# Optimization experiments

Hardware: AMD Instinct MI355X
Metric: run time of the kernel (lower is better)

The kernel has to match this reference:

```python
import jax, jax.numpy as jnp
import numpy as np

DIM = 1024
HEADS = 16
HEAD_DIM = DIM // HEADS
SCALE = 1.0 / np.sqrt(HEAD_DIM).astype(np.float32)


def setup_inputs() -> dict:
    key = jax.random.key(0)
    ks = jax.random.split(key, 5)
    B, N, C = 2, 2048, DIM
    x = jax.random.normal(ks[0], (B, N, C), dtype=jnp.float32)
    w_qkv = jax.random.normal(ks[1], (C, 3 * C), dtype=jnp.float32) * (1.0 / np.sqrt(C))
    b_qkv = jax.random.normal(ks[2], (3 * C,), dtype=jnp.float32) * 0.02
    w_proj = jax.random.normal(ks[3], (C, C), dtype=jnp.float32) * (1.0 / np.sqrt(C))
    b_proj = jax.random.normal(ks[4], (C,), dtype=jnp.float32) * 0.02
    return {"x": x, "w_qkv": w_qkv, "b_qkv": b_qkv, "w_proj": w_proj, "b_proj": b_proj}


def reference(x, w_qkv, b_qkv, w_proj, b_proj):
    B, N, C = x.shape
    H, D = HEADS, C // HEADS
    # fused QKV projection: [B,N,3C] -> [3,B,H,N,D]
    qkv = (x @ w_qkv + b_qkv).reshape(B, N, 3, H, D).transpose(2, 0, 3, 1, 4)
    q, k, v = qkv[0], qkv[1], qkv[2]
    # scores [B,H,N,N]
    scores = jnp.einsum("bhnd,bhmd->bhnm", q, k) * SCALE
    attn = jax.nn.softmax(scores, axis=-1)
    # attention output -> [B,N,C]
    y = jnp.einsum("bhnm,bhmd->bhnd", attn, v).transpose(0, 2, 1, 3).reshape(B, N, C)
    return y @ w_proj + b_proj
```

## Files before the change

kernel.cpp:

```cpp
#include <hip/hip_runtime.h>
#include <stdint.h>

typedef __attribute__((ext_vector_type(8))) short bf16x8;
typedef __attribute__((ext_vector_type(4))) float f32x4;
typedef __attribute__((ext_vector_type(4))) unsigned short us4;

#define DEV static __device__ __forceinline__

DEV unsigned short f2b(float f){
  union{float f; unsigned u;} x; x.f=f;
  unsigned r = x.u + 0x7fffu + ((x.u>>16)&1u);
  return (unsigned short)(r>>16);
}

DEV void glds16(const void* g, void* l){
  __builtin_amdgcn_global_load_lds((const __attribute__((address_space(1))) void*)g,
                                   (__attribute__((address_space(3))) void*)l, 16, 0, 0);
}

__global__ __launch_bounds__(256) void convert_k(const float* __restrict__ in,
                                                 unsigned short* __restrict__ out, int n){
  int i = (blockIdx.x*256 + threadIdx.x)*8;
  if(i >= n) return;
  f32x4 a = *(const f32x4*)(in + i);
  f32x4 b = *(const f32x4*)(in + i + 4);
  us4 o0, o1;
  o0.x=f2b(a[0]); o0.y=f2b(a[1]); o0.z=f2b(a[2]); o0.w=f2b(a[3]);
  o1.x=f2b(b[0]); o1.y=f2b(b[1]); o1.z=f2b(b[2]); o1.w=f2b(b[3]);
  *(us4*)(out + i) = o0;
  *(us4*)(out + i + 4) = o1;
}

__global__ __launch_bounds__(256) void transpose_k(const float* __restrict__ in,
                                                   unsigned short* __restrict__ out,
                                                   int ldin, int ldout){
  __shared__ __attribute__((aligned(16))) unsigned short tile[64][72];
  const int c0 = blockIdx.x*64, r0 = blockIdx.y*64;
  const int t = threadIdx.x;
  const int tr = t>>4, tc4 = (t&15)*4;
  #pragma unroll
  for(int j=0;j<4;j++){
    int r = tr + j*16;
    f32x4 v = *(const f32x4*)(in + (size_t)(r0+r)*ldin + c0 + tc4);
    tile[r][tc4+0] = f2b(v[0]);
    tile[r][tc4+1] = f2b(v[1]);
    tile[r][tc4+2] = f2b(v[2]);
    tile[r][tc4+3] = f2b(v[3]);
  }
  __syncthreads();
  #pragma unroll
  for(int j=0;j<4;j++){
    int r = tr + j*16;
    us4 v;
    v.x = tile[tc4+0][r];
    v.y = tile[tc4+1][r];
    v.z = tile[tc4+2][r];
    v.w = tile[tc4+3][r];
    *(us4*)(out + (size_t)(c0+r)*ldout + r0 + tc4) = v;
  }
}

__global__ __launch_bounds__(256) void vtrans_k(const unsigned short* __restrict__ in,
                                                unsigned short* __restrict__ out){
  __shared__ __attribute__((aligned(16))) unsigned short tile[64][72];
  const int n0 = blockIdx.x*64;
  const size_t base = (size_t)blockIdx.y*2048*64;
  const int t = threadIdx.x;
  const int tr = t>>4, tc4 = (t&15)*4;
  #pragma unroll
  for(int j=0;j<4;j++){
    int r = tr + j*16;
    *(us4*)&tile[r][tc4] = *(const us4*)(in + base + (size_t)(n0+r)*64 + tc4);
  }
  __syncthreads();
  #pragma unroll
  for(int j=0;j<4;j++){
    int r = tr + j*16;
    us4 v;
    v.x = tile[tc4+0][r];
    v.y = tile[tc4+1][r];
    v.z = tile[tc4+2][r];
    v.w = tile[tc4+3][r];
    *(us4*)(out + base + (size_t)r*2048 + n0 + tc4) = v;
  }
}

#define BK 64

DEV void gemm_core_128(const unsigned short* __restrict__ A,
                       const unsigned short* __restrict__ Bt,
                       int K, int rowA0, int rowB0,
                       unsigned short* As, unsigned short* Bs, f32x4 acc[4][4])
{
  const int t = threadIdx.x;
  const int lane = t & 63;
  const int wid  = t >> 6;
  const int wm = wid >> 1, wn = wid & 1;
  const f32x4 Z = {0.f,0.f,0.f,0.f};

  #pragma unroll
  for(int m=0;m<4;m++)
    #pragma unroll
    for(int n=0;n<4;n++) acc[m][n] = Z;

  for(int kt=0; kt<K; kt+=BK){
    __syncthreads();
    #pragma unroll
    for(int j=0;j<4;j++){
      int idx = t + 256*j;
      int row = idx >> 3;
      int ls  = (idx & 7) ^ (row & 7);
      glds16(A + (size_t)(rowA0 + row)*K + kt + ls*8, As + (size_t)(wid*64 + 256*j)*8);
    }
    #pragma unroll
    for(int j=0;j<4;j++){
      int idx = t + 256*j;
      int row = idx >> 3;
      int ls  = (idx & 7) ^ (row & 7);
      glds16(Bt + (size_t)(rowB0 + row)*K + kt + ls*8, Bs + (size_t)(wid*64 + 256*j)*8);
    }
    __syncthreads();
    #pragma unroll
    for(int ks=0; ks<2; ks++){
      bf16x8 af[4], bfr[4];
      #pragma unroll
      for(int m=0;m<4;m++){
        int row = wm*64 + m*16 + (lane&15);
        int sl  = (ks*4 + (lane>>4)) ^ (row&7);
        af[m] = *(const bf16x8*)(As + row*64 + sl*8);
      }
      #pragma unroll
      for(int n=0;n<4;n++){
        int row = wn*64 + n*16 + (lane&15);
        int sl  = (ks*4 + (lane>>4)) ^ (row&7);
        bfr[n] = *(const bf16x8*)(Bs + row*64 + sl*8);
      }
      #pragma unroll
      for(int m=0;m<4;m++)
        #pragma unroll
        for(int n=0;n<4;n++)
          acc[m][n] = __builtin_amdgcn_mfma_f32_16x16x32_bf16(af[m], bfr[n], acc[m][n], 0, 0, 0);
    }
  }
}

__global__ __launch_bounds__(256) void gemm_qkv(const unsigned short* __restrict__ xb,
                                                const unsigned short* __restrict__ Wt,
                                                const float* __restrict__ bqkv,
                                                unsigned short* __restrict__ q,
                                                unsigned short* __restrict__ k,
                                                unsigned short* __restrict__ v)
{
  __shared__ __attribute__((aligned(16))) unsigned short As[128*BK];
  __shared__ __attribute__((aligned(16))) unsigned short Bs[128*BK];
  f32x4 acc[4][4];
  const int bm = blockIdx.x, bn = blockIdx.y;
  gemm_core_128(xb, Wt, 1024, bm*128, bn*128, As, Bs, acc);

  const int t = threadIdx.x, lane = t&63, wid = t>>6, wm = wid>>1, wn = wid&1;
  #pragma unroll
  for(int m=0;m<4;m++)
    #pragma unroll
    for(int n=0;n<4;n++){
      int col = bn*128 + wn*64 + n*16 + (lane&15);
      float bias = bqkv[col];
      int three = col >> 10, h = (col>>6)&15, d = col&63;
      unsigned short* dst = (three==0) ? q : (three==1) ? k : v;
      #pragma unroll
      for(int r=0;r<4;r++){
        int row = bm*128 + wm*64 + m*16 + (lane>>4)*4 + r;
        int bb = row>>11, nn = row&2047;
        size_t bh = (size_t)(bb*16 + h);
        dst[(bh*2048 + nn)*64 + d] = f2b(acc[m][n][r] + bias);
      }
    }
}

__global__ __launch_bounds__(256) void gemm_proj(const unsigned short* __restrict__ y,
                                                 const unsigned short* __restrict__ Wt,
                                                 const float* __restrict__ bp,
                                                 float* __restrict__ out)
{
  __shared__ __attribute__((aligned(16))) unsigned short As[128*BK];
  __shared__ __attribute__((aligned(16))) unsigned short Bs[128*BK];
  f32x4 acc[4][4];
  const int bm = blockIdx.x, bn = blockIdx.y;
  gemm_core_128(y, Wt, 1024, bm*128, bn*128, As, Bs, acc);

  const int t = threadIdx.x, lane = t&63, wid = t>>6, wm = wid>>1, wn = wid&1;
  #pragma unroll
  for(int m=0;m<4;m++)
    #pragma unroll
    for(int n=0;n<4;n++){
      int col = bn*128 + wn*64 + n*16 + (lane&15);
      float bias = bp[col];
      #pragma unroll
      for(int r=0;r<4;r++){
        int row = bm*128 + wm*64 + m*16 + (lane>>4)*4 + r;
        out[(size_t)row*1024 + col] = acc[m][n][r] + bias;
      }
    }
}

__global__ __launch_bounds__(256, 4) void attn_k(const unsigned short* __restrict__ qg,
                                                 const unsigned short* __restrict__ kg,
                                                 const unsigned short* __restrict__ vtg,
                                                 unsigned short* __restrict__ y)
{
  __shared__ __attribute__((aligned(16))) unsigned short Ks[2][64*64];
  __shared__ __attribute__((aligned(16))) unsigned short VT[2][64*64];
  __shared__ __attribute__((aligned(16))) unsigned short Ps[4][16*64];

  const int bh = blockIdx.x;
  const int qt = blockIdx.y;
  const int b  = bh >> 4, h = bh & 15;
  const unsigned short* qh = qg  + (size_t)bh*2048*64;
  const unsigned short* kh = kg  + (size_t)bh*2048*64;
  const unsigned short* vh = vtg + (size_t)bh*64*2048;

  const int t = threadIdx.x, lane = t & 63, wid = t >> 6;
  const int q0 = qt*64 + wid*16;
  const int lq = lane & 15;
  const int lh = lane >> 4;
  const float C1 = 0.18033688011112042f;

  bf16x8 aq[2];
  #pragma unroll
  for(int ks=0;ks<2;ks++){
    int row = q0 + lq;
    aq[ks] = *(const bf16x8*)(qh + (size_t)row*64 + ks*32 + lh*8);
  }

  const f32x4 Z = {0.f,0.f,0.f,0.f};
  f32x4 accT[4];
  #pragma unroll
  for(int df=0;df<4;df++) accT[df] = Z;
  float lpart = 0.f;

  #pragma unroll
  for(int j=0;j<2;j++){
    int idx = t + 256*j;
    int row = idx >> 3;
    int ls  = (idx & 7) ^ (row & 7);
    glds16(kh + (size_t)row*64 + ls*8, &Ks[0][0] + (wid*64 + 256*j)*8);
    glds16(vh + (size_t)row*2048 + ls*8, &VT[0][0] + (wid*64 + 256*j)*8);
  }
  __syncthreads();

  for(int it=0; it<32; ++it){
    const int cur = it & 1, nxt = cur ^ 1;
    if(it < 31){
      int kvn = (it+1)*64;
      #pragma unroll
      for(int j=0;j<2;j++){
        int idx = t + 256*j;
        int row = idx >> 3;
        int ls  = (idx & 7) ^ (row & 7);
        glds16(kh + (size_t)(kvn+row)*64 + ls*8, &Ks[nxt][0] + (wid*64 + 256*j)*8);
        glds16(vh + (size_t)row*2048 + kvn + ls*8, &VT[nxt][0] + (wid*64 + 256*j)*8);
      }
    }

    f32x4 st[4];
    #pragma unroll
    for(int nc=0;nc<4;nc++) st[nc] = Z;
    __builtin_amdgcn_s_setprio(1);
    #pragma unroll
    for(int ks=0;ks<2;ks++){
      bf16x8 bk[4];
      #pragma unroll
      for(int nc=0;nc<4;nc++){
        int kvr = nc*16 + lq;
        int sl  = (ks*4 + lh) ^ (kvr&7);
        bk[nc] = *(const bf16x8*)(&Ks[cur][0] + kvr*64 + sl*8);
      }
      #pragma unroll
      for(int nc=0;nc<4;nc++)
        st[nc] = __builtin_amdgcn_mfma_f32_16x16x32_bf16(bk[nc], aq[ks], st[nc], 0,0,0);
    }
    __builtin_amdgcn_s_setprio(0);

    {
      float rs = 0.f;
      unsigned short* pr = &Ps[wid][0] + lq*64;
      #pragma unroll
      for(int nc=0;nc<4;nc++){
        float p0 = __builtin_amdgcn_exp2f(st[nc][0]*C1);
        float p1 = __builtin_amdgcn_exp2f(st[nc][1]*C1);
        float p2 = __builtin_amdgcn_exp2f(st[nc][2]*C1);
        float p3 = __builtin_amdgcn_exp2f(st[nc][3]*C1);
        rs += (p0+p1)+(p2+p3);
        unsigned w0, w1;
        asm("v_cvt_pk_bf16_f32 %0, %1, %2" : "=v"(w0) : "v"(p0), "v"(p1));
        asm("v_cvt_pk_bf16_f32 %0, %1, %2" : "=v"(w1) : "v"(p2), "v"(p3));
        int g    = 2*nc + (lh>>1);
        int phys = g ^ (lane&7);
        unsigned* dst = (unsigned*)(pr + phys*8 + (lh&1)*4);
        dst[0] = w0; dst[1] = w1;
      }
      lpart += rs;
    }

    __builtin_amdgcn_s_setprio(1);
    #pragma unroll
    for(int ks=0;ks<2;ks++){
      bf16x8 bv[4], pa;
      #pragma unroll
      for(int df=0;df<4;df++){
        int dr = df*16 + lq;
        int sl = (ks*4 + lh) ^ (dr&7);
        bv[df] = *(const bf16x8*)(&VT[cur][0] + dr*64 + sl*8);
      }
      {
        int g    = 4*ks + lh;
        int phys = g ^ (lane&7);
        pa = *(const bf16x8*)(&Ps[wid][0] + lq*64 + phys*8);
      }
      #pragma unroll
      for(int df=0;df<4;df++)
        accT[df] = __builtin_amdgcn_mfma_f32_16x16x32_bf16(bv[df], pa, accT[df], 0,0,0);
    }
    __builtin_amdgcn_s_setprio(0);

    __syncthreads();
  }

  float ls = lpart;
  ls += __shfl_xor(ls, 16, 64);
  ls += __shfl_xor(ls, 32, 64);
  float rl = 1.0f / ls;
  int row = q0 + lq;
  #pragma unroll
  for(int df=0;df<4;df++){
    us4 o;
    o.x = f2b(accT[df][0] * rl);
    o.y = f2b(accT[df][1] * rl);
    o.z = f2b(accT[df][2] * rl);
    o.w = f2b(accT[df][3] * rl);
    *(us4*)(y + ((size_t)b*2048 + row)*1024 + h*64 + df*16 + lh*4) = o;
  }
}

extern "C" void kernel_launch(void* const* d_in, const int* in_sizes, int n_in,
                              void* d_out, int out_size, void* d_ws, size_t ws_size,
                              hipStream_t stream) {
  const float* x     = (const float*)d_in[0];
  const float* wqkv  = (const float*)d_in[1];
  const float* bqkv  = (const float*)d_in[2];
  const float* wproj = (const float*)d_in[3];
  const float* bproj = (const float*)d_in[4];
  float* out = (float*)d_out;

  char* ws = (char*)d_ws;
  unsigned short* Wt1 = (unsigned short*)ws;  ws += (size_t)3072*1024*2;
  unsigned short* Wt2 = (unsigned short*)ws;  ws += (size_t)1024*1024*2;
  unsigned short* xb  = (unsigned short*)ws;  ws += (size_t)2*2048*1024*2;
  unsigned short* q   = (unsigned short*)ws;  ws += (size_t)2*16*2048*64*2;
  unsigned short* k   = (unsigned short*)ws;  ws += (size_t)2*16*2048*64*2;
  unsigned short* v   = (unsigned short*)ws;  ws += (size_t)2*16*2048*64*2;
  unsigned short* vt  = (unsigned short*)ws;  ws += (size_t)2*16*2048*64*2;
  unsigned short* y   = (unsigned short*)ws;  ws += (size_t)2*2048*1024*2;

  convert_k  <<<2048, 256, 0, stream>>>(x, xb, 2*2048*1024);
  transpose_k<<<dim3(48,16), 256, 0, stream>>>(wqkv,  Wt1, 3072, 1024);
  transpose_k<<<dim3(16,16), 256, 0, stream>>>(wproj, Wt2, 1024, 1024);
  gemm_qkv  <<<dim3(32,24), 256, 0, stream>>>(xb, Wt1, bqkv, q, k, v);
  vtrans_k  <<<dim3(32,32), 256, 0, stream>>>(v, vt);
  attn_k    <<<dim3(32,32), 256, 0, stream>>>(q, k, vt, y);
  gemm_proj <<<dim3(32, 8), 256, 0, stream>>>(y, Wt2, bproj, out);
}
```

Measured before the change: 137.9 us.

## Double-buffer GEMM LDS tiles with BK=32 to overlap global loads with MFMA

Rewrites the shared GEMM core used by the QKV and output projections to use two LDS buffers of K-depth 32 instead of one of depth 64. The next tile's global-to-LDS loads are issued before computing on the current tile, so memory latency overlaps with MFMA work, and each iteration needs one barrier instead of two. The XOR swizzle changes to match the 32-wide rows. In exchange there are twice as many iterations and barriers per K, and less compute per stage to hide each load behind. The glds loads are not explicitly waited on before the barrier, so correctness depends on the compiler inserting the vmcnt wait.

```diff
diff --git a/kernel.cpp b/kernel.cpp
--- a/kernel.cpp
+++ b/kernel.cpp
@@ -85,8 +85,6 @@
   }
 }
 
-#define BK 64
-
 DEV void gemm_core_128(const unsigned short* __restrict__ A,
                        const unsigned short* __restrict__ Bt,
                        int K, int rowA0, int rowB0,
@@ -96,6 +94,7 @@
   const int lane = t & 63;
   const int wid  = t >> 6;
   const int wm = wid >> 1, wn = wid & 1;
+  const int lh = lane >> 4;
   const f32x4 Z = {0.f,0.f,0.f,0.f};
 
   #pragma unroll
@@ -103,45 +102,48 @@
     #pragma unroll
     for(int n=0;n<4;n++) acc[m][n] = Z;
 
-  for(int kt=0; kt<K; kt+=BK){
+#define G_STAGE(kt, buf) do{                                                   \
+    _Pragma("unroll")                                                          \
+    for(int j=0;j<2;j++){                                                      \
+      int idx = t + 256*j;               \
+      int row = idx >> 2;                                                      \
+      int cl  = (idx & 3) ^ (row & 3);                                         \
+      glds16(A  + (size_t)(rowA0+row)*K + (kt) + cl*8,                         \
+             As + (buf)*4096 + (size_t)(wid*64 + 256*j)*8);                    \
+      glds16(Bt + (size_t)(rowB0+row)*K + (kt) + cl*8,                         \
+             Bs + (buf)*4096 + (size_t)(wid*64 + 256*j)*8);                    \
+    }}while(0)
+
+  G_STAGE(0, 0);
+  __syncthreads();
+
+  const int NT = K >> 5;
+  for(int tt=0; tt<NT; ++tt){
+    const int cur = tt & 1;
+    if(tt+1 < NT) G_STAGE((tt+1)*32, cur^1);
+
+    bf16x8 af[4], bfr[4];
+    #pragma unroll
+    for(int m=0;m<4;m++){
+      int row = wm*64 + m*16 + (lane&15);
+      int ph  = lh ^ (row&3);
+      af[m] = *(const bf16x8*)(As + cur*4096 + row*32 + ph*8);
+    }
+    #pragma unroll
+    for(int n=0;n<4;n++){
+      int row = wn*64 + n*16 + (lane&15);
+      int ph  = lh ^ (row&3);
+      bfr[n] = *(const bf16x8*)(Bs + cur*4096 + row*32 + ph*8);
+    }
+    #pragma unroll
+    for(int m=0;m<4;m++)
+      #pragma unroll
+      for(int n=0;n<4;n++)
+        acc[m][n] = __builtin_amdgcn_mfma_f32_16x16x32_bf16(af[m], bfr[n], acc[m][n], 0, 0, 0);
+
     __syncthreads();
-    #pragma unroll
-    for(int j=0;j<4;j++){
-      int idx = t + 256*j;
-      int row = idx >> 3;
-      int ls  = (idx & 7) ^ (row & 7);
-      glds16(A + (size_t)(rowA0 + row)*K + kt + ls*8, As + (size_t)(wid*64 + 256*j)*8);
-    }
-    #pragma unroll
-    for(int j=0;j<4;j++){
-      int idx = t + 256*j;
-      int row = idx >> 3;
-      int ls  = (idx & 7) ^ (row & 7);
-      glds16(Bt + (size_t)(rowB0 + row)*K + kt + ls*8, Bs + (size_t)(wid*64 + 256*j)*8);
-    }
-    __syncthreads();
-    #pragma unroll
-    for(int ks=0; ks<2; ks++){
-      bf16x8 af[4], bfr[4];
-      #pragma unroll
-      for(int m=0;m<4;m++){
-        int row = wm*64 + m*16 + (lane&15);
-        int sl  = (ks*4 + (lane>>4)) ^ (row&7);
-        af[m] = *(const bf16x8*)(As + row*64 + sl*8);
-      }
-      #pragma unroll
-      for(int n=0;n<4;n++){
-        int row = wn*64 + n*16 + (lane&15);
-        int sl  = (ks*4 + (lane>>4)) ^ (row&7);
-        bfr[n] = *(const bf16x8*)(Bs + row*64 + sl*8);
-      }
-      #pragma unroll
-      for(int m=0;m<4;m++)
-        #pragma unroll
-        for(int n=0;n<4;n++)
-          acc[m][n] = __builtin_amdgcn_mfma_f32_16x16x32_bf16(af[m], bfr[n], acc[m][n], 0, 0, 0);
-    }
-  }
+  }
+#undef G_STAGE
 }
 
 __global__ __launch_bounds__(256) void gemm_qkv(const unsigned short* __restrict__ xb,
@@ -151,8 +153,8 @@
                                                 unsigned short* __restrict__ k,
                                                 unsigned short* __restrict__ v)
 {
-  __shared__ __attribute__((aligned(16))) unsigned short As[128*BK];
-  __shared__ __attribute__((aligned(16))) unsigned short Bs[128*BK];
+  __shared__ __attribute__((aligned(16))) unsigned short As[2*128*32];
+  __shared__ __attribute__((aligned(16))) unsigned short Bs[2*128*32];
   f32x4 acc[4][4];
   const int bm = blockIdx.x, bn = blockIdx.y;
   gemm_core_128(xb, Wt, 1024, bm*128, bn*128, As, Bs, acc);
@@ -181,8 +183,8 @@
                                                  const float* __restrict__ bp,
                                                  float* __restrict__ out)
 {
-  __shared__ __attribute__((aligned(16))) unsigned short As[128*BK];
-  __shared__ __attribute__((aligned(16))) unsigned short Bs[128*BK];
+  __shared__ __attribute__((aligned(16))) unsigned short As[2*128*32];
+  __shared__ __attribute__((aligned(16))) unsigned short Bs[2*128*32];
   f32x4 acc[4][4];
   const int bm = blockIdx.x, bn = blockIdx.y;
   gemm_core_128(y, Wt, 1024, bm*128, bn*128, As, Bs, acc);
```

Result: slower. 142.0 us (+3.0%).
